# Kernel tuning notes

Measured on AMD Instinct MI355X. Metric: run time of the kernel, lower is better.

The kernel has to match this reference:

```python
import jax, jax.numpy as jnp
import numpy as np

N = 100000
E = 1600000
G = 2048          # number of graphs in the batch
HEADS = 4
HID = 16          # per-head channels
IN_CH = 128
D = HEADS * HID   # 64, concat output width per layer
NEG_SLOPE = 0.2


def _gat_layer(x, src, dst, W, a_src, a_dst, bias):
    # x: [N, Fin], W: [Fin, H*C], a_src/a_dst: [H, C], bias: [H*C]
    h = (x @ W).reshape(N, HEADS, HID)                      # [N, H, C]
    al_s = jnp.einsum('nhc,hc->nh', h, a_src)               # [N, H]
    al_d = jnp.einsum('nhc,hc->nh', h, a_dst)               # [N, H]
    e = jax.nn.leaky_relu(al_s[src] + al_d[dst], NEG_SLOPE) # [E+N, H]
    # segment softmax over incoming edges of each destination node
    m = jax.ops.segment_max(e, dst, num_segments=N)         # [N, H]
    e = jnp.exp(e - m[dst])
    s = jax.ops.segment_sum(e, dst, num_segments=N)
    alpha = e / (s[dst] + 1e-16)                            # [E+N, H]
    msg = h[src] * alpha[..., None]                         # [E+N, H, C]
    out = jax.ops.segment_sum(msg, dst, num_segments=N)     # [N, H, C]
    return out.reshape(N, D) + bias


def setup_inputs() -> dict:
    key = jax.random.key(0)
    ks = jax.random.split(key, 16)
    x = jax.random.normal(ks[0], (N, IN_CH), dtype=jnp.float32)
    edge_index = jax.random.randint(ks[1], (2, E), 0, N, dtype=jnp.int64)
    batch = jnp.sort(jax.random.randint(ks[2], (N,), 0, G, dtype=jnp.int64))
    inp = {'x': x, 'edge_index': edge_index, 'batch': batch}
    fins = [IN_CH, D, D]
    for i, fin in enumerate(fins):
        kk = jax.random.split(ks[3 + i], 4)
        sc = 1.0 / np.sqrt(fin)
        inp[f'W{i}'] = jax.random.normal(kk[0], (fin, D), dtype=jnp.float32) * sc
        inp[f'as{i}'] = jax.random.normal(kk[1], (HEADS, HID), dtype=jnp.float32) * 0.1
        inp[f'ad{i}'] = jax.random.normal(kk[2], (HEADS, HID), dtype=jnp.float32) * 0.1
        inp[f'b{i}'] = jnp.zeros((D,), dtype=jnp.float32)
    inp['head_w'] = jax.random.normal(ks[10], (1, D), dtype=jnp.float32) * (1.0 / np.sqrt(D))
    inp['head_b'] = jnp.zeros((1,), dtype=jnp.float32)
    return inp


def reference(x, edge_index, batch,
              W0, as0, ad0, b0,
              W1, as1, ad1, b1,
              W2, as2, ad2, b2,
              head_w, head_b):
    # PyG GATConv adds self-loops by default
    loops = jnp.arange(N, dtype=edge_index.dtype)
    src = jnp.concatenate([edge_index[0], loops])
    dst = jnp.concatenate([edge_index[1], loops])
    layers = [(W0, as0, ad0, b0), (W1, as1, ad1, b1), (W2, as2, ad2, b2)]
    h = x.astype(jnp.float32)
    for (W, a_s, a_d, b) in layers:
        h = _gat_layer(h, src, dst, W, a_s, a_d, b)
        h = jax.nn.relu(h)  # dropout p=0.0 -> identity
    pooled = jax.ops.segment_sum(h, batch, num_segments=G)  # [G, D]
    out = pooled @ head_w.T + head_b                         # [G, 1]
    return out.reshape(-1)                                   # out_dim == 1 -> flatten
```

## Files before the change

kernel.cpp:

```cpp
#include <hip/hip_runtime.h>
#include <hip/hip_bf16.h>
#include <hip/hip_fp16.h>
#include <cstdint>
#include <cstddef>

#define NN 100000
#define EE 1600000
#define GG 2048

constexpr int NB_SCAN = (NN + 255) / 256;

__device__ __forceinline__ float lrelu(float v) { return v > 0.f ? v : 0.2f * v; }

__global__ void k_count(const int* __restrict__ ei, int* __restrict__ deg,
                        int* __restrict__ rank) {
    int i = blockIdx.x * blockDim.x + threadIdx.x;
    if (i >= EE + NN) return;
    int d = (i < EE) ? ei[EE + i] : (i - EE);
    rank[i] = atomicAdd(&deg[d], 1);
}

__global__ void k_scan1(const int* __restrict__ deg, int* __restrict__ offs,
                        int* __restrict__ bsums) {
    __shared__ int tmp[256];
    int tid = threadIdx.x;
    int i = blockIdx.x * 256 + tid;
    int v = (i < NN) ? deg[i] : 0;
    tmp[tid] = v; __syncthreads();
    for (int off = 1; off < 256; off <<= 1) {
        int t = (tid >= off) ? tmp[tid - off] : 0;
        __syncthreads();
        tmp[tid] += t;
        __syncthreads();
    }
    if (i < NN) offs[i] = tmp[tid] - v;
    if (tid == 255) bsums[blockIdx.x] = tmp[255];
}

__global__ void k_scan2(int* __restrict__ bsums) {
    __shared__ int tmp[512];
    int tid = threadIdx.x;
    int v = (tid < NB_SCAN) ? bsums[tid] : 0;
    tmp[tid] = v; __syncthreads();
    for (int off = 1; off < 512; off <<= 1) {
        int t = (tid >= off) ? tmp[tid - off] : 0;
        __syncthreads();
        tmp[tid] += t;
        __syncthreads();
    }
    if (tid < NB_SCAN) bsums[tid] = tmp[tid] - v;
}

__global__ void k_scan3(int* __restrict__ offs, const int* __restrict__ bsums) {
    int i = blockIdx.x * 256 + threadIdx.x;
    if (i < NN) offs[i] += bsums[blockIdx.x];
}

__global__ void k_scatter(const int* __restrict__ ei, const int* __restrict__ offs,
                          const int* __restrict__ rank, int* __restrict__ col) {
    int i = blockIdx.x * blockDim.x + threadIdx.x;
    if (i >= EE + NN) return;
    int s, d;
    if (i < EE) { s = ei[i]; d = ei[EE + i]; } else { s = d = i - EE; }
    col[offs[d] + rank[i]] = s;
}

template <int FIN>
__global__ __launch_bounds__(256) void k_gemm(const float* __restrict__ X,
                                              const float* __restrict__ W,
                                              const float* __restrict__ asrc,
                                              const float* __restrict__ adst,
                                              float* __restrict__ H,
                                              float* __restrict__ als,
                                              float* __restrict__ ald) {
    int j  = threadIdx.x & 63;
    int ty = threadIdx.x >> 6;
    int row = __builtin_amdgcn_readfirstlane(blockIdx.x * 16 + ty * 4);
    const float* x0 = X + (size_t)row * FIN;
    const float* x1 = x0 + FIN;
    const float* x2 = x1 + FIN;
    const float* x3 = x2 + FIN;
    float a0 = 0.f, a1 = 0.f, a2 = 0.f, a3 = 0.f;
#pragma unroll
    for (int k = 0; k < FIN; k += 4) {
        float4 xa = *(const float4*)(x0 + k);
        float4 xb = *(const float4*)(x1 + k);
        float4 xc = *(const float4*)(x2 + k);
        float4 xd = *(const float4*)(x3 + k);
        float w0 = W[(k + 0) * 64 + j];
        float w1 = W[(k + 1) * 64 + j];
        float w2 = W[(k + 2) * 64 + j];
        float w3 = W[(k + 3) * 64 + j];
        a0 += xa.x * w0 + xa.y * w1 + xa.z * w2 + xa.w * w3;
        a1 += xb.x * w0 + xb.y * w1 + xb.z * w2 + xb.w * w3;
        a2 += xc.x * w0 + xc.y * w1 + xc.z * w2 + xc.w * w3;
        a3 += xd.x * w0 + xd.y * w1 + xd.z * w2 + xd.w * w3;
    }
    H[(size_t)(row + 0) * 64 + j] = a0;
    H[(size_t)(row + 1) * 64 + j] = a1;
    H[(size_t)(row + 2) * 64 + j] = a2;
    H[(size_t)(row + 3) * 64 + j] = a3;
    float asj = asrc[j], adj = adst[j];
    float accs[4] = {a0, a1, a2, a3};
#pragma unroll
    for (int r = 0; r < 4; r++) {
        float vs = accs[r] * asj;
        float vd = accs[r] * adj;
#pragma unroll
        for (int off = 8; off > 0; off >>= 1) {
            vs += __shfl_xor(vs, off, 64);
            vd += __shfl_xor(vd, off, 64);
        }
        if ((j & 15) == 0) {
            int h = j >> 4;
            als[(size_t)(row + r) * 4 + h] = vs;
            ald[(size_t)(row + r) * 4 + h] = vd;
        }
    }
}

__global__ __launch_bounds__(256, 6) void k_agg(
    const float* __restrict__ H, const float* __restrict__ als,
    const float* __restrict__ ald, const int* __restrict__ offs,
    const int* __restrict__ deg, const int* __restrict__ col,
    const float* __restrict__ bias, float* __restrict__ Hout,
    const int* __restrict__ batch, const float* __restrict__ hw,
    float* __restrict__ out, int last) {
    int tid = threadIdx.x;
    int g = tid >> 4;
    int l = tid & 15;
    int n = blockIdx.x * 16 + g;
    int start = offs[n];
    int len = deg[n];
    int hsel = l >> 2;
    float adh = ald[(size_t)n * 4 + hsel];
    const float4* Hp = (const float4*)H + l;

    float4 acc = {0.f, 0.f, 0.f, 0.f};
    float ssum = 0.f;

    for (int e = 0; e < len; e += 8) {
        bool  v[8];
        int   s[8];
#pragma unroll
        for (int i = 0; i < 8; i++) {
            v[i] = (e + i < len);
            s[i] = v[i] ? col[start + e + i] : 0;
        }
        float  w[8];
        float4 hr[8];
#pragma unroll
        for (int i = 0; i < 8; i++) {
            float a = als[(size_t)s[i] * 4 + hsel];
            hr[i] = Hp[(size_t)s[i] * 16];
            float ev = lrelu(a + adh);
            w[i] = v[i] ? __expf(ev) : 0.f;
        }
#pragma unroll
        for (int i = 0; i < 8; i++) {
            ssum  += w[i];
            acc.x = fmaf(w[i], hr[i].x, acc.x);
            acc.y = fmaf(w[i], hr[i].y, acc.y);
            acc.z = fmaf(w[i], hr[i].z, acc.z);
            acc.w = fmaf(w[i], hr[i].w, acc.w);
        }
    }
    float inv = 1.f / (ssum + 1e-16f);

    float4 b4 = ((const float4*)bias)[l];
    float4 o4;
    o4.x = fmaxf(acc.x * inv + b4.x, 0.f);
    o4.y = fmaxf(acc.y * inv + b4.y, 0.f);
    o4.z = fmaxf(acc.z * inv + b4.z, 0.f);
    o4.w = fmaxf(acc.w * inv + b4.w, 0.f);
    if (!last) {
        ((float4*)Hout)[(size_t)n * 16 + l] = o4;
    } else {
        float4 w4 = ((const float4*)hw)[l];
        float t = o4.x * w4.x + o4.y * w4.y + o4.z * w4.z + o4.w * w4.w;
#pragma unroll
        for (int off = 8; off > 0; off >>= 1) t += __shfl_xor(t, off, 16);
        if (l == 0) atomicAdd(&out[batch[n]], t);
    }
}

__global__ void k_out_init(const float* __restrict__ head_b, float* __restrict__ out) {
    int g = blockIdx.x * blockDim.x + threadIdx.x;
    if (g < GG) out[g] = head_b[0];
}

extern "C" void kernel_launch(void* const* d_in, const int* in_sizes, int n_in,
                              void* d_out, int out_size, void* d_ws, size_t ws_size,
                              hipStream_t stream) {
    const float* x     = (const float*)d_in[0];
    const int*   ei    = (const int*)d_in[1];
    const int*   batch = (const int*)d_in[2];
    const float* Wm[3] = {(const float*)d_in[3], (const float*)d_in[7],  (const float*)d_in[11]};
    const float* As[3] = {(const float*)d_in[4], (const float*)d_in[8],  (const float*)d_in[12]};
    const float* Ad[3] = {(const float*)d_in[5], (const float*)d_in[9],  (const float*)d_in[13]};
    const float* Bb[3] = {(const float*)d_in[6], (const float*)d_in[10], (const float*)d_in[14]};
    const float* hw = (const float*)d_in[15];
    const float* hb = (const float*)d_in[16];
    float* out = (float*)d_out;

    uint8_t* w = (uint8_t*)d_ws;
    auto alloc = [&](size_t bytes) -> void* {
        void* p = (void*)w;
        w += (bytes + 255) & ~(size_t)255;
        return p;
    };
    float* H       = (float*)alloc((size_t)NN * 64 * 4);
    float* Bf      = (float*)alloc((size_t)NN * 64 * 4);
    float* als     = (float*)alloc((size_t)NN * 4 * 4);
    float* ald     = (float*)alloc((size_t)NN * 4 * 4);
    int*   deg     = (int*)alloc((size_t)NN * 4);
    int*   offs    = (int*)alloc((size_t)NN * 4);
    int*   rank    = (int*)alloc((size_t)(EE + NN) * 4);
    int*   col     = (int*)alloc((size_t)(EE + NN) * 4);
    int*   bsums   = (int*)alloc((size_t)((NB_SCAN + 63) & ~63) * 4);

    hipMemsetAsync(deg, 0, (size_t)NN * 4, stream);

    int eb = (EE + NN + 255) / 256;
    k_count  <<<eb, 256, 0, stream>>>(ei, deg, rank);
    k_scan1  <<<NB_SCAN, 256, 0, stream>>>(deg, offs, bsums);
    k_scan2  <<<1, 512, 0, stream>>>(bsums);
    k_scan3  <<<NB_SCAN, 256, 0, stream>>>(offs, bsums);
    k_scatter<<<eb, 256, 0, stream>>>(ei, offs, rank, col);
    k_out_init<<<(GG + 255) / 256, 256, 0, stream>>>(hb, out);

    const float* cur_in = x;
    for (int L = 0; L < 3; L++) {
        if (L == 0)
            k_gemm<128><<<NN / 16, 256, 0, stream>>>(
                cur_in, Wm[L], As[L], Ad[L], H, als, ald);
        else
            k_gemm<64><<<NN / 16, 256, 0, stream>>>(
                cur_in, Wm[L], As[L], Ad[L], H, als, ald);
        k_agg <<<NN / 16, 256, 0, stream>>>(
            H, als, ald, offs, deg, col, Bb[L], Bf, batch, hw, out, (L == 2) ? 1 : 0);
        cur_in = Bf;
    }
}
```

Before: 546.8 us.

## Fuse next-layer GEMM into aggregation and replace three-pass scan with wave-atomic offsets

Each non-final aggregation kernel now also multiplies its output rows by the next layer's weight matrix, which is staged in shared memory, and computes the next attention logits. This removes two standalone GEMM launches and the write and re-read of intermediate features. The three scan kernels and the output init are replaced by a single kernel that scans within each wave and claims space with an atomic cursor. CSR segments therefore land in arbitrary order, which can cost locality. The 16KB+ of shared memory per block and the dropped launch_bounds occupancy hint may reduce occupancy of the gather-heavy aggregation.

```diff
diff --git a/kernel.cpp b/kernel.cpp
--- a/kernel.cpp
+++ b/kernel.cpp
@@ -7,8 +7,6 @@
 #define NN 100000
 #define EE 1600000
 #define GG 2048
-
-constexpr int NB_SCAN = (NN + 255) / 256;
 
 __device__ __forceinline__ float lrelu(float v) { return v > 0.f ? v : 0.2f * v; }
 
@@ -20,40 +18,24 @@
     rank[i] = atomicAdd(&deg[d], 1);
 }
 
-__global__ void k_scan1(const int* __restrict__ deg, int* __restrict__ offs,
-                        int* __restrict__ bsums) {
-    __shared__ int tmp[256];
-    int tid = threadIdx.x;
-    int i = blockIdx.x * 256 + tid;
-    int v = (i < NN) ? deg[i] : 0;
-    tmp[tid] = v; __syncthreads();
-    for (int off = 1; off < 256; off <<= 1) {
-        int t = (tid >= off) ? tmp[tid - off] : 0;
-        __syncthreads();
-        tmp[tid] += t;
-        __syncthreads();
-    }
-    if (i < NN) offs[i] = tmp[tid] - v;
-    if (tid == 255) bsums[blockIdx.x] = tmp[255];
-}
-
-__global__ void k_scan2(int* __restrict__ bsums) {
-    __shared__ int tmp[512];
-    int tid = threadIdx.x;
-    int v = (tid < NB_SCAN) ? bsums[tid] : 0;
-    tmp[tid] = v; __syncthreads();
-    for (int off = 1; off < 512; off <<= 1) {
-        int t = (tid >= off) ? tmp[tid - off] : 0;
-        __syncthreads();
-        tmp[tid] += t;
-        __syncthreads();
-    }
-    if (tid < NB_SCAN) bsums[tid] = tmp[tid] - v;
-}
-
-__global__ void k_scan3(int* __restrict__ offs, const int* __restrict__ bsums) {
-    int i = blockIdx.x * 256 + threadIdx.x;
-    if (i < NN) offs[i] += bsums[blockIdx.x];
+__global__ void k_alloc(const int* __restrict__ deg, int* __restrict__ offs,
+                        int* __restrict__ cursor, const float* __restrict__ head_b,
+                        float* __restrict__ out) {
+    int i = blockIdx.x * blockDim.x + threadIdx.x;
+    int lane = threadIdx.x & 63;
+    int d = (i < NN) ? deg[i] : 0;
+    int incl = d;
+#pragma unroll
+    for (int off = 1; off < 64; off <<= 1) {
+        int t = __shfl_up(incl, off, 64);
+        if (lane >= off) incl += t;
+    }
+    int total = __shfl(incl, 63, 64);
+    int base = 0;
+    if (lane == 63) base = atomicAdd(cursor, total);
+    base = __shfl(base, 63, 64);
+    if (i < NN) offs[i] = base + incl - d;
+    if (i < GG) out[i] = head_b[0];
 }
 
 __global__ void k_scatter(const int* __restrict__ ei, const int* __restrict__ offs,
@@ -119,13 +101,17 @@
     }
 }
 
-__global__ __launch_bounds__(256, 6) void k_agg(
+__global__ __launch_bounds__(256) void k_aggf(
     const float* __restrict__ H, const float* __restrict__ als,
     const float* __restrict__ ald, const int* __restrict__ offs,
     const int* __restrict__ deg, const int* __restrict__ col,
-    const float* __restrict__ bias, float* __restrict__ Hout,
-    const int* __restrict__ batch, const float* __restrict__ hw,
-    float* __restrict__ out, int last) {
+    const float* __restrict__ bias,
+    const float* __restrict__ W,
+    const float* __restrict__ asrc,
+    const float* __restrict__ adst,
+    float* __restrict__ Hn, float* __restrict__ alsn, float* __restrict__ aldn) {
+    __shared__ float wl[4096];
+    __shared__ float xs[16 * 68];
     int tid = threadIdx.x;
     int g = tid >> 4;
     int l = tid & 15;
@@ -136,9 +122,12 @@
     float adh = ald[(size_t)n * 4 + hsel];
     const float4* Hp = (const float4*)H + l;
 
+#pragma unroll
+    for (int t = 0; t < 4; t++)
+        ((float4*)wl)[tid + t * 256] = ((const float4*)W)[tid + t * 256];
+
     float4 acc = {0.f, 0.f, 0.f, 0.f};
     float ssum = 0.f;
-
     for (int e = 0; e < len; e += 8) {
         bool  v[8];
         int   s[8];
@@ -166,27 +155,99 @@
         }
     }
     float inv = 1.f / (ssum + 1e-16f);
-
     float4 b4 = ((const float4*)bias)[l];
-    float4 o4;
-    o4.x = fmaxf(acc.x * inv + b4.x, 0.f);
-    o4.y = fmaxf(acc.y * inv + b4.y, 0.f);
-    o4.z = fmaxf(acc.z * inv + b4.z, 0.f);
-    o4.w = fmaxf(acc.w * inv + b4.w, 0.f);
-    if (!last) {
-        ((float4*)Hout)[(size_t)n * 16 + l] = o4;
-    } else {
-        float4 w4 = ((const float4*)hw)[l];
-        float t = o4.x * w4.x + o4.y * w4.y + o4.z * w4.z + o4.w * w4.w;
-#pragma unroll
-        for (int off = 8; off > 0; off >>= 1) t += __shfl_xor(t, off, 16);
-        if (l == 0) atomicAdd(&out[batch[n]], t);
-    }
-}
-
-__global__ void k_out_init(const float* __restrict__ head_b, float* __restrict__ out) {
-    int g = blockIdx.x * blockDim.x + threadIdx.x;
-    if (g < GG) out[g] = head_b[0];
+    float* xr = xs + g * 68 + 4 * l;
+    xr[0] = fmaxf(acc.x * inv + b4.x, 0.f);
+    xr[1] = fmaxf(acc.y * inv + b4.y, 0.f);
+    xr[2] = fmaxf(acc.z * inv + b4.z, 0.f);
+    xr[3] = fmaxf(acc.w * inv + b4.w, 0.f);
+
+    __syncthreads();
+
+    float4 o = {0.f, 0.f, 0.f, 0.f};
+    const float* xrow = xs + g * 68;
+    const float* wcol = wl + 4 * l;
+#pragma unroll
+    for (int k = 0; k < 64; k += 4) {
+        float4 xv = *(const float4*)(xrow + k);
+        float4 w0 = *(const float4*)(wcol + (k + 0) * 64);
+        float4 w1 = *(const float4*)(wcol + (k + 1) * 64);
+        float4 w2 = *(const float4*)(wcol + (k + 2) * 64);
+        float4 w3 = *(const float4*)(wcol + (k + 3) * 64);
+        o.x += xv.x * w0.x + xv.y * w1.x + xv.z * w2.x + xv.w * w3.x;
+        o.y += xv.x * w0.y + xv.y * w1.y + xv.z * w2.y + xv.w * w3.y;
+        o.z += xv.x * w0.z + xv.y * w1.z + xv.z * w2.z + xv.w * w3.z;
+        o.w += xv.x * w0.w + xv.y * w1.w + xv.z * w2.w + xv.w * w3.w;
+    }
+    ((float4*)Hn)[(size_t)n * 16 + l] = o;
+
+    float4 av = ((const float4*)asrc)[l];
+    float4 dv = ((const float4*)adst)[l];
+    float vs = o.x * av.x + o.y * av.y + o.z * av.z + o.w * av.w;
+    float vd = o.x * dv.x + o.y * dv.y + o.z * dv.z + o.w * dv.w;
+    vs += __shfl_xor(vs, 1, 16); vs += __shfl_xor(vs, 2, 16);
+    vd += __shfl_xor(vd, 1, 16); vd += __shfl_xor(vd, 2, 16);
+    if ((l & 3) == 0) {
+        int h = l >> 2;
+        alsn[(size_t)n * 4 + h] = vs;
+        aldn[(size_t)n * 4 + h] = vd;
+    }
+}
+
+__global__ __launch_bounds__(256) void k_aggl(
+    const float* __restrict__ H, const float* __restrict__ als,
+    const float* __restrict__ ald, const int* __restrict__ offs,
+    const int* __restrict__ deg, const int* __restrict__ col,
+    const float* __restrict__ bias, const int* __restrict__ batch,
+    const float* __restrict__ hw, float* __restrict__ out) {
+    int tid = threadIdx.x;
+    int g = tid >> 4;
+    int l = tid & 15;
+    int n = blockIdx.x * 16 + g;
+    int start = offs[n];
+    int len = deg[n];
+    int hsel = l >> 2;
+    float adh = ald[(size_t)n * 4 + hsel];
+    const float4* Hp = (const float4*)H + l;
+
+    float4 acc = {0.f, 0.f, 0.f, 0.f};
+    float ssum = 0.f;
+    for (int e = 0; e < len; e += 8) {
+        bool  v[8];
+        int   s[8];
+#pragma unroll
+        for (int i = 0; i < 8; i++) {
+            v[i] = (e + i < len);
+            s[i] = v[i] ? col[start + e + i] : 0;
+        }
+        float  w[8];
+        float4 hr[8];
+#pragma unroll
+        for (int i = 0; i < 8; i++) {
+            float a = als[(size_t)s[i] * 4 + hsel];
+            hr[i] = Hp[(size_t)s[i] * 16];
+            float ev = lrelu(a + adh);
+            w[i] = v[i] ? __expf(ev) : 0.f;
+        }
+#pragma unroll
+        for (int i = 0; i < 8; i++) {
+            ssum  += w[i];
+            acc.x = fmaf(w[i], hr[i].x, acc.x);
+            acc.y = fmaf(w[i], hr[i].y, acc.y);
+            acc.z = fmaf(w[i], hr[i].z, acc.z);
+            acc.w = fmaf(w[i], hr[i].w, acc.w);
+        }
+    }
+    float inv = 1.f / (ssum + 1e-16f);
+    float4 b4 = ((const float4*)bias)[l];
+    float4 w4 = ((const float4*)hw)[l];
+    float t = fmaxf(acc.x * inv + b4.x, 0.f) * w4.x
+            + fmaxf(acc.y * inv + b4.y, 0.f) * w4.y
+            + fmaxf(acc.z * inv + b4.z, 0.f) * w4.z
+            + fmaxf(acc.w * inv + b4.w, 0.f) * w4.w;
+#pragma unroll
+    for (int off = 8; off > 0; off >>= 1) t += __shfl_xor(t, off, 16);
+    if (l == 0) atomicAdd(&out[batch[n]], t);
 }
 
 extern "C" void kernel_launch(void* const* d_in, const int* in_sizes, int n_in,
@@ -209,36 +270,31 @@
         w += (bytes + 255) & ~(size_t)255;
         return p;
     };
-    float* H       = (float*)alloc((size_t)NN * 64 * 4);
-    float* Bf      = (float*)alloc((size_t)NN * 64 * 4);
-    float* als     = (float*)alloc((size_t)NN * 4 * 4);
-    float* ald     = (float*)alloc((size_t)NN * 4 * 4);
-    int*   deg     = (int*)alloc((size_t)NN * 4);
-    int*   offs    = (int*)alloc((size_t)NN * 4);
-    int*   rank    = (int*)alloc((size_t)(EE + NN) * 4);
-    int*   col     = (int*)alloc((size_t)(EE + NN) * 4);
-    int*   bsums   = (int*)alloc((size_t)((NB_SCAN + 63) & ~63) * 4);
-
-    hipMemsetAsync(deg, 0, (size_t)NN * 4, stream);
+    float* H    = (float*)alloc((size_t)NN * 64 * 4);
+    float* Bf   = (float*)alloc((size_t)NN * 64 * 4);
+    float* als  = (float*)alloc((size_t)NN * 4 * 4);
+    float* ald  = (float*)alloc((size_t)NN * 4 * 4);
+    float* als2 = (float*)alloc((size_t)NN * 4 * 4);
+    float* ald2 = (float*)alloc((size_t)NN * 4 * 4);
+    int*   deg  = (int*)alloc((size_t)(NN + 64) * 4);
+    int*   offs = (int*)alloc((size_t)NN * 4);
+    int*   rank = (int*)alloc((size_t)(EE + NN) * 4);
+    int*   col  = (int*)alloc((size_t)(EE + NN) * 4);
+    int*   cursor = deg + NN;
+
+    hipMemsetAsync(deg, 0, (size_t)(NN + 1) * 4, stream);
 
     int eb = (EE + NN + 255) / 256;
+    int nb = (NN + 255) / 256;
     k_count  <<<eb, 256, 0, stream>>>(ei, deg, rank);
-    k_scan1  <<<NB_SCAN, 256, 0, stream>>>(deg, offs, bsums);
-    k_scan2  <<<1, 512, 0, stream>>>(bsums);
-    k_scan3  <<<NB_SCAN, 256, 0, stream>>>(offs, bsums);
+    k_alloc  <<<nb, 256, 0, stream>>>(deg, offs, cursor, hb, out);
     k_scatter<<<eb, 256, 0, stream>>>(ei, offs, rank, col);
-    k_out_init<<<(GG + 255) / 256, 256, 0, stream>>>(hb, out);
-
-    const float* cur_in = x;
-    for (int L = 0; L < 3; L++) {
-        if (L == 0)
-            k_gemm<128><<<NN / 16, 256, 0, stream>>>(
-                cur_in, Wm[L], As[L], Ad[L], H, als, ald);
-        else
-            k_gemm<64><<<NN / 16, 256, 0, stream>>>(
-                cur_in, Wm[L], As[L], Ad[L], H, als, ald);
-        k_agg <<<NN / 16, 256, 0, stream>>>(
-            H, als, ald, offs, deg, col, Bb[L], Bf, batch, hw, out, (L == 2) ? 1 : 0);
-        cur_in = Bf;
-    }
-}
+
+    k_gemm<128><<<NN / 16, 256, 0, stream>>>(x, Wm[0], As[0], Ad[0], H, als, ald);
+    k_aggf<<<NN / 16, 256, 0, stream>>>(H,  als,  ald,  offs, deg, col, Bb[0],
+                                        Wm[1], As[1], Ad[1], Bf, als2, ald2);
+    k_aggf<<<NN / 16, 256, 0, stream>>>(Bf, als2, ald2, offs, deg, col, Bb[1],
+                                        Wm[2], As[2], Ad[2], H, als, ald);
+    k_aggl<<<NN / 16, 256, 0, stream>>>(H,  als,  ald,  offs, deg, col, Bb[2],
+                                        batch, hw, out);
+}
```

Measured after the change: 528.1 us. -3.4%, faster.

## Partition edges by source octant and phase aggregation for L2 locality

Applied to the files above, without the earlier changes.

Builds a CSR where each destination's incoming edges are bucketed into 8 source-node ranges, replacing the scan kernels with a warp-scan plus atomic cursor allocation. The aggregation kernel becomes persistent (1024 blocks, 7 nodes per group) and walks the 8 source slices in phases, with a loose cross-block barrier and prefetch, so the gathered H rows for a slice stay resident in L2. Edge counting is also fused with the first GEMM in one launch, and output init is folded into the allocation kernel. In exchange the edge order within a destination is no longer deterministic, and the spin barrier with bounded polling adds sync overhead and register pressure from 7 accumulator slots.

```diff
diff --git a/kernel.cpp b/kernel.cpp
--- a/kernel.cpp
+++ b/kernel.cpp
@@ -8,74 +8,30 @@
 #define EE 1600000
 #define GG 2048
 
-constexpr int NB_SCAN = (NN + 255) / 256;
+#define NOCT 8
+#define OCTW 12500
+#define SLICE_BYTES (OCTW * 256)
+#define NBLK_AGG 1024
+#define NGRP (NBLK_AGG * 16)
+#define NSLOT 7
+#define PFCHUNK (SLICE_BYTES / 128)
+
+constexpr int NB_CNT = (EE + NN + 255) / 256;
+constexpr int NB_GEMM = NN / 16;
 
 __device__ __forceinline__ float lrelu(float v) { return v > 0.f ? v : 0.2f * v; }
 
-__global__ void k_count(const int* __restrict__ ei, int* __restrict__ deg,
-                        int* __restrict__ rank) {
-    int i = blockIdx.x * blockDim.x + threadIdx.x;
-    if (i >= EE + NN) return;
-    int d = (i < EE) ? ei[EE + i] : (i - EE);
-    rank[i] = atomicAdd(&deg[d], 1);
-}
-
-__global__ void k_scan1(const int* __restrict__ deg, int* __restrict__ offs,
-                        int* __restrict__ bsums) {
-    __shared__ int tmp[256];
-    int tid = threadIdx.x;
-    int i = blockIdx.x * 256 + tid;
-    int v = (i < NN) ? deg[i] : 0;
-    tmp[tid] = v; __syncthreads();
-    for (int off = 1; off < 256; off <<= 1) {
-        int t = (tid >= off) ? tmp[tid - off] : 0;
-        __syncthreads();
-        tmp[tid] += t;
-        __syncthreads();
-    }
-    if (i < NN) offs[i] = tmp[tid] - v;
-    if (tid == 255) bsums[blockIdx.x] = tmp[255];
-}
-
-__global__ void k_scan2(int* __restrict__ bsums) {
-    __shared__ int tmp[512];
-    int tid = threadIdx.x;
-    int v = (tid < NB_SCAN) ? bsums[tid] : 0;
-    tmp[tid] = v; __syncthreads();
-    for (int off = 1; off < 512; off <<= 1) {
-        int t = (tid >= off) ? tmp[tid - off] : 0;
-        __syncthreads();
-        tmp[tid] += t;
-        __syncthreads();
-    }
-    if (tid < NB_SCAN) bsums[tid] = tmp[tid] - v;
-}
-
-__global__ void k_scan3(int* __restrict__ offs, const int* __restrict__ bsums) {
-    int i = blockIdx.x * 256 + threadIdx.x;
-    if (i < NN) offs[i] += bsums[blockIdx.x];
-}
-
-__global__ void k_scatter(const int* __restrict__ ei, const int* __restrict__ offs,
-                          const int* __restrict__ rank, int* __restrict__ col) {
-    int i = blockIdx.x * blockDim.x + threadIdx.x;
-    if (i >= EE + NN) return;
-    int s, d;
-    if (i < EE) { s = ei[i]; d = ei[EE + i]; } else { s = d = i - EE; }
-    col[offs[d] + rank[i]] = s;
-}
-
 template <int FIN>
-__global__ __launch_bounds__(256) void k_gemm(const float* __restrict__ X,
-                                              const float* __restrict__ W,
-                                              const float* __restrict__ asrc,
-                                              const float* __restrict__ adst,
-                                              float* __restrict__ H,
-                                              float* __restrict__ als,
-                                              float* __restrict__ ald) {
+__device__ __forceinline__ void gemm_body(int bidx, const float* __restrict__ X,
+                                          const float* __restrict__ W,
+                                          const float* __restrict__ asrc,
+                                          const float* __restrict__ adst,
+                                          float* __restrict__ H,
+                                          float* __restrict__ als,
+                                          float* __restrict__ ald) {
     int j  = threadIdx.x & 63;
     int ty = threadIdx.x >> 6;
-    int row = __builtin_amdgcn_readfirstlane(blockIdx.x * 16 + ty * 4);
+    int row = __builtin_amdgcn_readfirstlane(bidx * 16 + ty * 4);
     const float* x0 = X + (size_t)row * FIN;
     const float* x1 = x0 + FIN;
     const float* x2 = x1 + FIN;
@@ -119,74 +75,187 @@
     }
 }
 
-__global__ __launch_bounds__(256, 6) void k_agg(
+template <int FIN>
+__global__ __launch_bounds__(256) void k_gemm(const float* __restrict__ X,
+                                              const float* __restrict__ W,
+                                              const float* __restrict__ asrc,
+                                              const float* __restrict__ adst,
+                                              float* __restrict__ H,
+                                              float* __restrict__ als,
+                                              float* __restrict__ ald) {
+    gemm_body<FIN>(blockIdx.x, X, W, asrc, adst, H, als, ald);
+}
+
+__global__ __launch_bounds__(256) void k_cg(const int* __restrict__ ei,
+                                            int* __restrict__ deg2,
+                                            int* __restrict__ rank2,
+                                            const float* __restrict__ X,
+                                            const float* __restrict__ W,
+                                            const float* __restrict__ asrc,
+                                            const float* __restrict__ adst,
+                                            float* __restrict__ H,
+                                            float* __restrict__ als,
+                                            float* __restrict__ ald) {
+    if (blockIdx.x < NB_CNT) {
+        int i = blockIdx.x * 256 + threadIdx.x;
+        if (i < EE + NN) {
+            int s, d;
+            if (i < EE) { s = ei[i]; d = ei[EE + i]; } else { s = d = i - EE; }
+            unsigned oct = (unsigned)s / OCTW;
+            rank2[i] = atomicAdd(&deg2[d * 8 + oct], 1);
+        }
+    } else {
+        gemm_body<128>(blockIdx.x - NB_CNT, X, W, asrc, adst, H, als, ald);
+    }
+}
+
+__global__ void k_alloc2(const int* __restrict__ deg2, int* __restrict__ starts,
+                         int* __restrict__ cursor, const float* __restrict__ head_b,
+                         float* __restrict__ out) {
+    int i = blockIdx.x * 256 + threadIdx.x;
+    int lane = threadIdx.x & 63;
+    int rel[8];
+    int tot = 0;
+    if (i < NN) {
+#pragma unroll
+        for (int o = 0; o < 8; o++) { rel[o] = tot; tot += deg2[i * 8 + o]; }
+    }
+    int incl = tot;
+#pragma unroll
+    for (int off = 1; off < 64; off <<= 1) {
+        int t = __shfl_up(incl, off, 64);
+        if (lane >= off) incl += t;
+    }
+    int wtot = __shfl(incl, 63, 64);
+    int base = 0;
+    if (lane == 63) base = atomicAdd(cursor, wtot);
+    base = __shfl(base, 63, 64);
+    int mybase = base + incl - tot;
+    if (i < NN) {
+#pragma unroll
+        for (int o = 0; o < 8; o++) starts[i * 8 + o] = mybase + rel[o];
+    }
+    if (i < GG) out[i] = head_b[0];
+}
+
+__global__ void k_scatter2(const int* __restrict__ ei, const int* __restrict__ starts,
+                           const int* __restrict__ rank2, int* __restrict__ col) {
+    int i = blockIdx.x * blockDim.x + threadIdx.x;
+    if (i >= EE + NN) return;
+    int s, d;
+    if (i < EE) { s = ei[i]; d = ei[EE + i]; } else { s = d = i - EE; }
+    unsigned oct = (unsigned)s / OCTW;
+    col[starts[d * 8 + oct] + rank2[i]] = s;
+}
+
+__global__ __launch_bounds__(256, 4) void k_aggp(
     const float* __restrict__ H, const float* __restrict__ als,
-    const float* __restrict__ ald, const int* __restrict__ offs,
-    const int* __restrict__ deg, const int* __restrict__ col,
-    const float* __restrict__ bias, float* __restrict__ Hout,
-    const int* __restrict__ batch, const float* __restrict__ hw,
-    float* __restrict__ out, int last) {
+    const float* __restrict__ ald, const int* __restrict__ starts,
+    const int* __restrict__ cnts, const int* __restrict__ col,
+    const float* __restrict__ bias, const int* __restrict__ batch,
+    const float* __restrict__ hw, float* __restrict__ out,
+    float* __restrict__ Hout, int* __restrict__ ctr, int last) {
     int tid = threadIdx.x;
+    int b = blockIdx.x;
     int g = tid >> 4;
     int l = tid & 15;
-    int n = blockIdx.x * 16 + g;
-    int start = offs[n];
-    int len = deg[n];
     int hsel = l >> 2;
-    float adh = ald[(size_t)n * 4 + hsel];
+    int gid = b * 16 + g;
+    int rid = b >> 3;
     const float4* Hp = (const float4*)H + l;
 
-    float4 acc = {0.f, 0.f, 0.f, 0.f};
-    float ssum = 0.f;
-
-    for (int e = 0; e < len; e += 8) {
-        bool  v[8];
-        int   s[8];
-#pragma unroll
-        for (int i = 0; i < 8; i++) {
-            v[i] = (e + i < len);
-            s[i] = v[i] ? col[start + e + i] : 0;
-        }
-        float  w[8];
-        float4 hr[8];
-#pragma unroll
-        for (int i = 0; i < 8; i++) {
-            float a = als[(size_t)s[i] * 4 + hsel];
-            hr[i] = Hp[(size_t)s[i] * 16];
-            float ev = lrelu(a + adh);
-            w[i] = v[i] ? __expf(ev) : 0.f;
-        }
-#pragma unroll
-        for (int i = 0; i < 8; i++) {
-            ssum  += w[i];
-            acc.x = fmaf(w[i], hr[i].x, acc.x);
-            acc.y = fmaf(w[i], hr[i].y, acc.y);
-            acc.z = fmaf(w[i], hr[i].z, acc.z);
-            acc.w = fmaf(w[i], hr[i].w, acc.w);
-        }
-    }
-    float inv = 1.f / (ssum + 1e-16f);
+    float4 acc[NSLOT];
+    float ssum[NSLOT];
+    float adh[NSLOT];
+#pragma unroll
+    for (int t = 0; t < NSLOT; t++) {
+        acc[t] = make_float4(0.f, 0.f, 0.f, 0.f);
+        ssum[t] = 0.f;
+        int n = gid + t * NGRP;
+        adh[t] = (n < NN) ? ald[(size_t)n * 4 + hsel] : 0.f;
+    }
+
+    for (int p = 0; p < NOCT; p++) {
+        __syncthreads();
+        if (tid == 0) {
+            __hip_atomic_fetch_add(&ctr[p], 1, __ATOMIC_RELAXED, __HIP_MEMORY_SCOPE_AGENT);
+            int polls = 0;
+            while (polls++ < 64 &&
+                   __hip_atomic_load(&ctr[p], __ATOMIC_RELAXED, __HIP_MEMORY_SCOPE_AGENT) < NBLK_AGG)
+                __builtin_amdgcn_s_sleep(1);
+        }
+        __syncthreads();
+
+        {
+            const char* sb = (const char*)H + (size_t)p * SLICE_BYTES + (size_t)rid * PFCHUNK;
+            int o0 = tid * 64;
+            int o1 = 16384 + tid * 64;
+            float pf0 = (o0 < PFCHUNK) ? *(const float*)(sb + o0) : 0.f;
+            float pf1 = (o1 < PFCHUNK) ? *(const float*)(sb + o1) : 0.f;
+            asm volatile("" :: "v"(pf0), "v"(pf1));
+        }
+
+#pragma unroll
+        for (int t = 0; t < NSLOT; t++) {
+            int n = gid + t * NGRP;
+            if (n < NN) {
+                int sidx = n * 8 + p;
+                int st = starts[sidx];
+                int c  = cnts[sidx];
+                int e = st, end = st + c;
+                float ad = adh[t];
+                for (; e + 2 <= end; e += 2) {
+                    int s0 = col[e], s1 = col[e + 1];
+                    float a0 = als[(size_t)s0 * 4 + hsel];
+                    float a1 = als[(size_t)s1 * 4 + hsel];
+                    float4 h0 = Hp[(size_t)s0 * 16];
+                    float4 h1 = Hp[(size_t)s1 * 16];
+                    float w0 = __expf(lrelu(a0 + ad));
+                    float w1 = __expf(lrelu(a1 + ad));
+                    ssum[t] += w0 + w1;
+                    acc[t].x = fmaf(w0, h0.x, fmaf(w1, h1.x, acc[t].x));
+                    acc[t].y = fmaf(w0, h0.y, fmaf(w1, h1.y, acc[t].y));
+                    acc[t].z = fmaf(w0, h0.z, fmaf(w1, h1.z, acc[t].z));
+                    acc[t].w = fmaf(w0, h0.w, fmaf(w1, h1.w, acc[t].w));
+                }
+                if (e < end) {
+                    int s0 = col[e];
+                    float a0 = als[(size_t)s0 * 4 + hsel];
+                    float4 h0 = Hp[(size_t)s0 * 16];
+                    float w0 = __expf(lrelu(a0 + ad));
+                    ssum[t] += w0;
+                    acc[t].x = fmaf(w0, h0.x, acc[t].x);
+                    acc[t].y = fmaf(w0, h0.y, acc[t].y);
+                    acc[t].z = fmaf(w0, h0.z, acc[t].z);
+                    acc[t].w = fmaf(w0, h0.w, acc[t].w);
+                }
+            }
+        }
+    }
 
     float4 b4 = ((const float4*)bias)[l];
-    float4 o4;
-    o4.x = fmaxf(acc.x * inv + b4.x, 0.f);
-    o4.y = fmaxf(acc.y * inv + b4.y, 0.f);
-    o4.z = fmaxf(acc.z * inv + b4.z, 0.f);
-    o4.w = fmaxf(acc.w * inv + b4.w, 0.f);
-    if (!last) {
-        ((float4*)Hout)[(size_t)n * 16 + l] = o4;
-    } else {
-        float4 w4 = ((const float4*)hw)[l];
-        float t = o4.x * w4.x + o4.y * w4.y + o4.z * w4.z + o4.w * w4.w;
-#pragma unroll
-        for (int off = 8; off > 0; off >>= 1) t += __shfl_xor(t, off, 16);
-        if (l == 0) atomicAdd(&out[batch[n]], t);
-    }
-}
-
-__global__ void k_out_init(const float* __restrict__ head_b, float* __restrict__ out) {
-    int g = blockIdx.x * blockDim.x + threadIdx.x;
-    if (g < GG) out[g] = head_b[0];
+    float4 w4 = make_float4(0.f, 0.f, 0.f, 0.f);
+    if (last) w4 = ((const float4*)hw)[l];
+#pragma unroll
+    for (int t = 0; t < NSLOT; t++) {
+        int n = gid + t * NGRP;
+        if (n < NN) {
+            float inv = 1.f / (ssum[t] + 1e-16f);
+            float4 o;
+            o.x = fmaxf(acc[t].x * inv + b4.x, 0.f);
+            o.y = fmaxf(acc[t].y * inv + b4.y, 0.f);
+            o.z = fmaxf(acc[t].z * inv + b4.z, 0.f);
+            o.w = fmaxf(acc[t].w * inv + b4.w, 0.f);
+            if (!last) {
+                ((float4*)Hout)[(size_t)n * 16 + l] = o;
+            } else {
+                float tt = o.x * w4.x + o.y * w4.y + o.z * w4.z + o.w * w4.w;
+#pragma unroll
+                for (int off = 8; off > 0; off >>= 1) tt += __shfl_xor(tt, off, 16);
+                if (l == 0) atomicAdd(&out[batch[n]], tt);
+            }
+        }
+    }
 }
 
 extern "C" void kernel_launch(void* const* d_in, const int* in_sizes, int n_in,
@@ -209,36 +278,33 @@
         w += (bytes + 255) & ~(size_t)255;
         return p;
     };
-    float* H       = (float*)alloc((size_t)NN * 64 * 4);
-    float* Bf      = (float*)alloc((size_t)NN * 64 * 4);
-    float* als     = (float*)alloc((size_t)NN * 4 * 4);
-    float* ald     = (float*)alloc((size_t)NN * 4 * 4);
-    int*   deg     = (int*)alloc((size_t)NN * 4);
-    int*   offs    = (int*)alloc((size_t)NN * 4);
-    int*   rank    = (int*)alloc((size_t)(EE + NN) * 4);
-    int*   col     = (int*)alloc((size_t)(EE + NN) * 4);
-    int*   bsums   = (int*)alloc((size_t)((NB_SCAN + 63) & ~63) * 4);
-
-    hipMemsetAsync(deg, 0, (size_t)NN * 4, stream);
+    float* H     = (float*)alloc((size_t)NN * 64 * 4);
+    float* Bf    = (float*)alloc((size_t)NN * 64 * 4);
+    float* als   = (float*)alloc((size_t)NN * 4 * 4);
+    float* ald   = (float*)alloc((size_t)NN * 4 * 4);
+    int*   meta  = (int*)alloc(((size_t)NN * 8 + 64) * 4);
+    int*   starts= (int*)alloc((size_t)NN * 8 * 4);
+    int*   rank2 = (int*)alloc((size_t)(EE + NN) * 4);
+    int*   col   = (int*)alloc((size_t)(EE + NN) * 4);
+
+    int* deg2   = meta;
+    int* cursor = meta + (size_t)NN * 8;
+    int* ctr    = cursor + 8;
+
+    hipMemsetAsync(meta, 0, ((size_t)NN * 8 + 64) * 4, stream);
 
     int eb = (EE + NN + 255) / 256;
-    k_count  <<<eb, 256, 0, stream>>>(ei, deg, rank);
-    k_scan1  <<<NB_SCAN, 256, 0, stream>>>(deg, offs, bsums);
-    k_scan2  <<<1, 512, 0, stream>>>(bsums);
-    k_scan3  <<<NB_SCAN, 256, 0, stream>>>(offs, bsums);
-    k_scatter<<<eb, 256, 0, stream>>>(ei, offs, rank, col);
-    k_out_init<<<(GG + 255) / 256, 256, 0, stream>>>(hb, out);
-
-    const float* cur_in = x;
-    for (int L = 0; L < 3; L++) {
-        if (L == 0)
-            k_gemm<128><<<NN / 16, 256, 0, stream>>>(
-                cur_in, Wm[L], As[L], Ad[L], H, als, ald);
-        else
-            k_gemm<64><<<NN / 16, 256, 0, stream>>>(
-                cur_in, Wm[L], As[L], Ad[L], H, als, ald);
-        k_agg <<<NN / 16, 256, 0, stream>>>(
-            H, als, ald, offs, deg, col, Bb[L], Bf, batch, hw, out, (L == 2) ? 1 : 0);
-        cur_in = Bf;
-    }
-}
+    k_cg<<<NB_CNT + NB_GEMM, 256, 0, stream>>>(ei, deg2, rank2,
+                                               x, Wm[0], As[0], Ad[0], H, als, ald);
+    k_alloc2<<<(NN + 255) / 256, 256, 0, stream>>>(deg2, starts, cursor, hb, out);
+    k_scatter2<<<eb, 256, 0, stream>>>(ei, starts, rank2, col);
+
+    k_aggp<<<NBLK_AGG, 256, 0, stream>>>(H, als, ald, starts, deg2, col, Bb[0],
+                                         batch, hw, out, Bf, ctr + 0, 0);
+    k_gemm<64><<<NB_GEMM, 256, 0, stream>>>(Bf, Wm[1], As[1], Ad[1], H, als, ald);
+    k_aggp<<<NBLK_AGG, 256, 0, stream>>>(H, als, ald, starts, deg2, col, Bb[1],
+                                         batch, hw, out, Bf, ctr + 8, 0);
+    k_gemm<64><<<NB_GEMM, 256, 0, stream>>>(Bf, Wm[2], As[2], Ad[2], H, als, ald);
+    k_aggp<<<NBLK_AGG, 256, 0, stream>>>(H, als, ald, starts, deg2, col, Bb[2],
+                                         batch, hw, out, H , ctr + 16, 1);
+}
```

New measurement: 1.848 ms. 238% more time.
